# Optimization experiments

Measured on AMD Instinct MI355X. Metric: run time of the kernel, lower is better.

The kernel has to match this reference:

```python
import jax, jax.numpy as jnp
import numpy as np

B, S = 4096, 128
POS_RANK, DIR_RANK = 10, 4
WIDTH = 256
POS_DIM = POS_RANK * 6  # 60
DIR_DIM = DIR_RANK * 6  # 24
SKIPS = (4,)


def _pe(x, rank):
    # x: [N, 3] -> [N, 6*rank]; sin/cos of x scaled by 2^i for i in 0..rank-1
    freqs = (2.0 ** jnp.arange(rank)).astype(x.dtype)        # [L]
    xf = x[..., None] * freqs                                 # [N, 3, L]
    enc = jnp.concatenate([jnp.sin(xf), jnp.cos(xf)], axis=-1)  # [N, 3, 2L]
    return enc.reshape(x.shape[0], -1)


def _linear_init(key, fan_in, fan_out):
    k1, k2 = jax.random.split(key)
    bound = 1.0 / np.sqrt(fan_in)
    W = jax.random.uniform(k1, (fan_in, fan_out), jnp.float32, -bound, bound)
    b = jax.random.uniform(k2, (fan_out,), jnp.float32, -bound, bound)
    return W, b


def setup_inputs() -> dict:
    key = jax.random.key(0)
    ks = jax.random.split(key, 16)
    inp = {
        "input_pos": jax.random.normal(ks[0], (B, S, 3), jnp.float32),
        "input_dir": jax.random.normal(ks[1], (B, S, 3), jnp.float32),
    }
    # trunk layers: in-dims follow skip-concat structure
    in_dims = [POS_DIM] + [WIDTH + POS_DIM if (i in SKIPS) else WIDTH for i in range(7)]
    for i, d_in in enumerate(in_dims):
        W, b = _linear_init(ks[2 + i], d_in, WIDTH)
        inp[f"W{i}"] = W
        inp[f"b{i}"] = b
    inp["Wd"], inp["bd"] = _linear_init(ks[10], WIDTH, 1)
    inp["Wc0"], inp["bc0"] = _linear_init(ks[11], WIDTH + DIR_DIM, WIDTH // 2)
    inp["Wc1"], inp["bc1"] = _linear_init(ks[12], WIDTH // 2, 3)
    return inp


def reference(input_pos, input_dir,
              W0, b0, W1, b1, W2, b2, W3, b3, W4, b4, W5, b5, W6, b6, W7, b7,
              Wd, bd, Wc0, bc0, Wc1, bc1):
    Ws = [W0, W1, W2, W3, W4, W5, W6, W7]
    bs = [b0, b1, b2, b3, b4, b5, b6, b7]
    b, s, _ = input_pos.shape
    embed_pos = _pe(input_pos.reshape(-1, 3), POS_RANK)  # [N, 60]
    embed_dir = _pe(input_dir.reshape(-1, 3), DIR_RANK)  # [N, 24]
    hx = embed_pos
    for i, (W, bb) in enumerate(zip(Ws, bs)):
        hx = jax.nn.relu(hx @ W + bb)
        if i in SKIPS:
            hx = jnp.concatenate([hx, embed_pos], axis=1)
    density = (hx @ Wd + bd).reshape(b, s)
    dir_feat = jnp.concatenate([hx, embed_dir], axis=1)  # [N, 280]
    color = (jax.nn.relu(dir_feat @ Wc0 + bc0) @ Wc1 + bc1).reshape(b, s, 3)
    return density, color
```

## Files before the change

kernel.cpp:

```cpp
#include <hip/hip_runtime.h>
#include <hip/hip_bf16.h>

using bf16 = __bf16;
typedef __bf16 bf16x8 __attribute__((ext_vector_type(8)));
typedef __bf16 bf16x4 __attribute__((ext_vector_type(4)));
typedef float  f32x4  __attribute__((ext_vector_type(4)));

#define MFMA16(a, b, c) __builtin_amdgcn_mfma_f32_16x16x32_bf16((a), (b), (c), 0, 0, 0)

constexpr int P0  = 0;
constexpr int P1  = 16384;
constexpr int P2  = 81920;
constexpr int P3  = 147456;
constexpr int P4  = 212992;
constexpr int P5  = 278528;
constexpr int P6  = 360448;
constexpr int P7  = 425984;
constexpr int PD  = 491520;
constexpr int PC0 = 495616;
constexpr int PC1 = 532480;

constexpr int NPTS = 4096 * 128;
constexpr int MT = 128;
constexpr int PTILES = MT / 16;
constexpr int SH = 320;


struct PackArgs {
    const float* src[11];
    int K[11], N[11], Ntiles[11], tasks[11], dstoff[11];
};

__global__ void nerf_pack(PackArgs pa, bf16* __restrict__ dst) {
    int idx = blockIdx.x * 256 + threadIdx.x;
    for (int l = 0; l < 11; ++l) {
        if (idx < pa.tasks[l]) {
            const int lane = idx & 63;
            const int blk  = idx >> 6;
            const int nt   = blk % pa.Ntiles[l];
            const int kt   = blk / pa.Ntiles[l];
            const int kb   = kt * 32 + (lane >> 4) * 8;
            const int n    = nt * 16 + (lane & 15);
            const float* s = pa.src[l];
            const int K = pa.K[l], N = pa.N[l];
            bf16x8 v;
#pragma unroll
            for (int j = 0; j < 8; ++j) {
                int k = kb + j;
                v[j] = (bf16)((k < K && n < N) ? s[(size_t)k * N + n] : 0.f);
            }
            *(bf16x8*)(dst + pa.dstoff[l] + (size_t)idx * 8) = v;
            return;
        }
        idx -= pa.tasks[l];
    }
}

template <int KP, int N, bool RELU, int MODE, bool HAZARD, int COFF>
__device__ __forceinline__ void layer(bf16* H,
                                      const bf16* __restrict__ wp,
                                      const float* __restrict__ bias,
                                      float* __restrict__ gout, int m0) {
    constexpr int NW     = 8;
    constexpr int NTILES = N / 16;
    constexpr int NT_W   = (NTILES >= 16) ? 4 : ((NTILES >= 8) ? 2 : 1);
    constexpr int CG     = NTILES / NT_W;
    static_assert(CG <= NW && NW % CG == 0, "wave split");
    constexpr int NPG    = NW / CG;
    constexpr int PT_W   = PTILES / NPG;

    const int tid  = threadIdx.x;
    const int lane = tid & 63;
    const int w    = tid >> 6;
    const int l15  = lane & 15;
    const int quad = lane >> 4;
    const int swz  = l15 & 7;
    const int nt0  = (w % CG) * NT_W;
    const int pt0  = (w / CG) * PT_W;

    f32x4 acc[PT_W][NT_W];
    if constexpr (MODE == 0) {
#pragma unroll
        for (int nt = 0; nt < NT_W; ++nt) {
            f32x4 b4 = *(const f32x4*)(bias + (nt0 + nt) * 16 + quad * 4);
#pragma unroll
            for (int pt = 0; pt < PT_W; ++pt) acc[pt][nt] = b4;
        }
    } else if constexpr (MODE == 1) {
        const float bv = bias[0];
        f32x4 t = {bv, bv, bv, bv};
#pragma unroll
        for (int pt = 0; pt < PT_W; ++pt) acc[pt][0] = t;
    } else {
        f32x4 t = {bias[0], bias[1], bias[2], 0.f};
#pragma unroll
        for (int pt = 0; pt < PT_W; ++pt) acc[pt][0] = t;
    }

#pragma unroll 2
    for (int kt = 0; kt < KP / 32; ++kt) {
        bf16x8 wf[NT_W];
#pragma unroll
        for (int nt = 0; nt < NT_W; ++nt)
            wf[nt] = *(const bf16x8*)(wp + ((size_t)(kt * NTILES + nt0 + nt) * 64 + lane) * 8);
#pragma unroll
        for (int pt = 0; pt < PT_W; ++pt) {
            const int point = (pt0 + pt) * 16 + l15;
            const int chunk = (COFF >> 3) + kt * 4 + quad;
            bf16x8 af = *(const bf16x8*)(H + point * SH + ((chunk ^ swz) << 3));
#pragma unroll
            for (int nt = 0; nt < NT_W; ++nt)
                acc[pt][nt] = MFMA16(wf[nt], af, acc[pt][nt]);
        }
    }
    if (HAZARD) __syncthreads();

    if constexpr (MODE == 0) {
#pragma unroll
        for (int pt = 0; pt < PT_W; ++pt) {
            const int point = (pt0 + pt) * 16 + l15;
#pragma unroll
            for (int nt = 0; nt < NT_W; ++nt) {
                f32x4 a = acc[pt][nt];
                bf16x4 o;
#pragma unroll
                for (int r = 0; r < 4; ++r) {
                    float v = a[r];
                    if (RELU) v = v > 0.f ? v : 0.f;
                    o[r] = (bf16)v;
                }
                const int chunk = (nt0 + nt) * 2 + (quad >> 1);
                *(bf16x4*)(H + point * SH + ((chunk ^ swz) << 3) + (quad & 1) * 4) = o;
            }
        }
        __syncthreads();
    } else if constexpr (MODE == 1) {
        if (quad == 0) {
#pragma unroll
            for (int pt = 0; pt < PT_W; ++pt)
                gout[m0 + (pt0 + pt) * 16 + l15] = acc[pt][0][0];
        }
    } else {
        if (quad == 0) {
#pragma unroll
            for (int pt = 0; pt < PT_W; ++pt) {
                const size_t p3 = (size_t)(m0 + (pt0 + pt) * 16 + l15) * 3;
                gout[p3 + 0] = acc[pt][0][0];
                gout[p3 + 1] = acc[pt][0][1];
                gout[p3 + 2] = acc[pt][0][2];
            }
        }
    }
}

__global__ __launch_bounds__(512, 4)
void nerf_main(const float* __restrict__ pos, const float* __restrict__ dir,
               const float* __restrict__ b0, const float* __restrict__ b1,
               const float* __restrict__ b2, const float* __restrict__ b3,
               const float* __restrict__ b4, const float* __restrict__ b5,
               const float* __restrict__ b6, const float* __restrict__ b7,
               const float* __restrict__ bd, const float* __restrict__ bc0,
               const float* __restrict__ bc1,
               const bf16* __restrict__ wpk, float* __restrict__ out) {
    __shared__ __align__(16) bf16 H[MT * SH];

    const int m0 = blockIdx.x * MT;
    const int tid = threadIdx.x;

    {
        const int row = tid >> 2;
        const int sub = tid & 3;
        const int swz = row & 7;
        const size_t pb = (size_t)(m0 + row) * 3;
        float xs[3] = { pos[pb], pos[pb + 1], pos[pb + 2] };
#pragma unroll
        for (int h = 0; h < 2; ++h) {
            const int chunk = 32 + sub * 2 + h;
            bf16* dst = H + row * SH + ((chunk ^ swz) << 3);
#pragma unroll
            for (int j = 0; j < 8; ++j) {
                const int col = sub * 16 + h * 8 + j;
                float v = 0.f;
                if (col < 60) {
                    const int c = col / 20, rem = col % 20, s = rem / 10, i = rem % 10;
                    const float arg = xs[c] * (float)(1 << i);
                    v = s ? __cosf(arg) : __sinf(arg);
                }
                dst[j] = (bf16)v;
            }
        }
    }
    __syncthreads();

    layer<64,  256, true, 0, false, 256>(H, wpk + P0, b0, nullptr, m0);
    layer<256, 256, true, 0, true,  0  >(H, wpk + P1, b1, nullptr, m0);
    layer<256, 256, true, 0, true,  0  >(H, wpk + P2, b2, nullptr, m0);
    layer<256, 256, true, 0, true,  0  >(H, wpk + P3, b3, nullptr, m0);
    layer<256, 256, true, 0, true,  0  >(H, wpk + P4, b4, nullptr, m0);
    layer<320, 256, true, 0, true,  0  >(H, wpk + P5, b5, nullptr, m0);
    layer<256, 256, true, 0, true,  0  >(H, wpk + P6, b6, nullptr, m0);
    layer<256, 256, true, 0, true,  0  >(H, wpk + P7, b7, nullptr, m0);

    layer<256, 16, false, 1, false, 0>(H, wpk + PD, bd, out, m0);

    {
        const int row = tid >> 2;
        const int sub = tid & 3;
        const int swz = row & 7;
        const size_t db = (size_t)(m0 + row) * 3;
        float ds[3] = { dir[db], dir[db + 1], dir[db + 2] };
        const int chunk = 32 + sub;
        bf16* dst = H + row * SH + ((chunk ^ swz) << 3);
#pragma unroll
        for (int j = 0; j < 8; ++j) {
            const int col = sub * 8 + j;
            float v = 0.f;
            if (col < 24) {
                const int c = col / 8, rem = col % 8, s = rem / 4, i = rem % 4;
                const float arg = ds[c] * (float)(1 << i);
                v = s ? __cosf(arg) : __sinf(arg);
            }
            dst[j] = (bf16)v;
        }
    }
    __syncthreads();

    layer<288, 128, true, 0, true,  0>(H, wpk + PC0, bc0, nullptr, m0);
    layer<128, 16, false, 2, false, 0>(H, wpk + PC1, bc1, out + NPTS, m0);
}

__global__ void nerf_sentinel(float* __restrict__ out, float val) {
    if (threadIdx.x == 0 && blockIdx.x == 0) out[0] = val;
}

extern "C" void kernel_launch(void* const* d_in, const int* in_sizes, int n_in,
                              void* d_out, int out_size, void* d_ws, size_t ws_size,
                              hipStream_t stream) {
    static const int exp2[24] = {
        1572864, 1572864,
        15360, 256, 65536, 256, 65536, 256, 65536, 256,
        65536, 256, 80896, 256, 65536, 256, 65536, 256,
        256, 1, 35840, 128, 384, 3
    };
    int bad = -1;
    if (n_in != 24) bad = 99;
    else {
        for (int i = 0; i < 24; ++i)
            if (in_sizes[i] != exp2[i]) { bad = i; break; }
    }
    if (bad < 0 && out_size != NPTS * 4) bad = 97;
    if (bad >= 0) {
        nerf_sentinel<<<1, 64, 0, stream>>>((float*)d_out, 20000.f + 100.f * bad);
        return;
    }

    static const int wi[11] = {2, 4, 6, 8, 10, 12, 14, 16, 18, 20, 22};
    static const int Ks[11] = {60, 256, 256, 256, 256, 316, 256, 256, 256, 280, 128};
    static const int Ns[11] = {256, 256, 256, 256, 256, 256, 256, 256, 1, 128, 3};
    static const int Kp[11] = {64, 256, 256, 256, 256, 320, 256, 256, 256, 288, 128};
    static const int Np[11] = {256, 256, 256, 256, 256, 256, 256, 256, 16, 128, 16};

    PackArgs pa;
    int off = 0, total_tasks = 0;
    for (int l = 0; l < 11; ++l) {
        pa.src[l]    = (const float*)d_in[wi[l]];
        pa.K[l]      = Ks[l];
        pa.N[l]      = Ns[l];
        pa.Ntiles[l] = Np[l] / 16;
        pa.tasks[l]  = (Kp[l] / 32) * (Np[l] / 16) * 64;
        pa.dstoff[l] = off;
        off += pa.tasks[l] * 8;
        total_tasks += pa.tasks[l];
    }
    bf16* wpk = (bf16*)d_ws;

    nerf_pack<<<(total_tasks + 255) / 256, 256, 0, stream>>>(pa, wpk);

    nerf_main<<<NPTS / MT, 512, 0, stream>>>(
        (const float*)d_in[0], (const float*)d_in[1],
        (const float*)d_in[3], (const float*)d_in[5], (const float*)d_in[7],
        (const float*)d_in[9], (const float*)d_in[11], (const float*)d_in[13],
        (const float*)d_in[15], (const float*)d_in[17], (const float*)d_in[19],
        (const float*)d_in[21], (const float*)d_in[23],
        wpk, (float*)d_out);
}
```

Baseline: 586.0 us.

## Switch MLP layers from 16x16x32 to 32x32x16 bf16 MFMA tiles

Replaces the 16x16x32 MFMA with the 32x32x16 variant throughout the fused NeRF MLP. The weight packing, LDS fragment addressing, swizzle, bias initialisation and output write-back are reworked for 32-wide tiles. The larger instruction should reuse each loaded operand fragment across more output elements, cutting LDS and global fragment loads per FLOP. The costs are more accumulator registers per wave (16 floats per tile), idle waves in the narrow output layers, and a tricky swizzle scheme that has to stay consistent between the read and write paths.

```diff
diff --git a/kernel.cpp b/kernel.cpp
--- a/kernel.cpp
+++ b/kernel.cpp
@@ -5,8 +5,9 @@
 typedef __bf16 bf16x8 __attribute__((ext_vector_type(8)));
 typedef __bf16 bf16x4 __attribute__((ext_vector_type(4)));
 typedef float  f32x4  __attribute__((ext_vector_type(4)));
-
-#define MFMA16(a, b, c) __builtin_amdgcn_mfma_f32_16x16x32_bf16((a), (b), (c), 0, 0, 0)
+typedef float  f32x16 __attribute__((ext_vector_type(16)));
+
+#define MFMA32(a, b, c) __builtin_amdgcn_mfma_f32_32x32x16_bf16((a), (b), (c), 0, 0, 0)
 
 constexpr int P0  = 0;
 constexpr int P1  = 16384;
@@ -17,12 +18,12 @@
 constexpr int P6  = 360448;
 constexpr int P7  = 425984;
 constexpr int PD  = 491520;
-constexpr int PC0 = 495616;
-constexpr int PC1 = 532480;
+constexpr int PC0 = 499712;
+constexpr int PC1 = 536576;
 
 constexpr int NPTS = 4096 * 128;
 constexpr int MT = 128;
-constexpr int PTILES = MT / 16;
+constexpr int PTILES = MT / 32;
 constexpr int SH = 320;
 
 
@@ -39,8 +40,8 @@
             const int blk  = idx >> 6;
             const int nt   = blk % pa.Ntiles[l];
             const int kt   = blk / pa.Ntiles[l];
-            const int kb   = kt * 32 + (lane >> 4) * 8;
-            const int n    = nt * 16 + (lane & 15);
+            const int kb   = kt * 16 + ((lane >> 5) << 3);
+            const int n    = nt * 32 + (lane & 31);
             const float* s = pa.src[l];
             const int K = pa.K[l], N = pa.N[l];
             bf16x8 v;
@@ -61,56 +62,68 @@
                                       const bf16* __restrict__ wp,
                                       const float* __restrict__ bias,
                                       float* __restrict__ gout, int m0) {
-    constexpr int NW     = 8;
-    constexpr int NTILES = N / 16;
-    constexpr int NT_W   = (NTILES >= 16) ? 4 : ((NTILES >= 8) ? 2 : 1);
+    constexpr int NTILES = N / 32;
+    constexpr int NT_W   = (NTILES >= 2) ? 2 : 1;
     constexpr int CG     = NTILES / NT_W;
-    static_assert(CG <= NW && NW % CG == 0, "wave split");
-    constexpr int NPG    = NW / CG;
-    constexpr int PT_W   = PTILES / NPG;
+    constexpr int NPG    = 8 / CG;
+    constexpr int PT_W   = (PTILES + NPG - 1) / NPG;
+    constexpr int CB     = COFF >> 3;
 
     const int tid  = threadIdx.x;
     const int lane = tid & 63;
     const int w    = tid >> 6;
-    const int l15  = lane & 15;
-    const int quad = lane >> 4;
-    const int swz  = l15 & 7;
+    const int l31  = lane & 31;
+    const int hi   = lane >> 5;
     const int nt0  = (w % CG) * NT_W;
     const int pt0  = (w / CG) * PT_W;
-
-    f32x4 acc[PT_W][NT_W];
+    const int s15  = l31 & 15, s7 = l31 & 7;
+
+    f32x16 acc[PT_W][NT_W];
     if constexpr (MODE == 0) {
 #pragma unroll
         for (int nt = 0; nt < NT_W; ++nt) {
-            f32x4 b4 = *(const f32x4*)(bias + (nt0 + nt) * 16 + quad * 4);
-#pragma unroll
-            for (int pt = 0; pt < PT_W; ++pt) acc[pt][nt] = b4;
-        }
-    } else if constexpr (MODE == 1) {
-        const float bv = bias[0];
-        f32x4 t = {bv, bv, bv, bv};
-#pragma unroll
-        for (int pt = 0; pt < PT_W; ++pt) acc[pt][0] = t;
+#pragma unroll
+            for (int g = 0; g < 4; ++g) {
+                f32x4 b4 = *(const f32x4*)(bias + (nt0 + nt) * 32 + g * 8 + hi * 4);
+#pragma unroll
+                for (int pt = 0; pt < PT_W; ++pt) {
+                    acc[pt][nt][g * 4 + 0] = b4[0];
+                    acc[pt][nt][g * 4 + 1] = b4[1];
+                    acc[pt][nt][g * 4 + 2] = b4[2];
+                    acc[pt][nt][g * 4 + 3] = b4[3];
+                }
+            }
+        }
     } else {
-        f32x4 t = {bias[0], bias[1], bias[2], 0.f};
-#pragma unroll
-        for (int pt = 0; pt < PT_W; ++pt) acc[pt][0] = t;
-    }
-
-#pragma unroll 2
-    for (int kt = 0; kt < KP / 32; ++kt) {
+#pragma unroll
+        for (int pt = 0; pt < PT_W; ++pt)
+#pragma unroll
+            for (int r = 0; r < 16; ++r) {
+                const int chan = (r & 3) + 8 * (r >> 2) + 4 * hi;
+                float bv = 0.f;
+                if (MODE == 1) bv = (chan == 0) ? bias[0] : 0.f;
+                else           bv = (chan < 3) ? bias[chan] : 0.f;
+                acc[pt][0][r] = bv;
+            }
+    }
+
+#pragma unroll 4
+    for (int kt = 0; kt < KP / 16; ++kt) {
         bf16x8 wf[NT_W];
 #pragma unroll
         for (int nt = 0; nt < NT_W; ++nt)
             wf[nt] = *(const bf16x8*)(wp + ((size_t)(kt * NTILES + nt0 + nt) * 64 + lane) * 8);
+        const int c = CB + kt * 2 + hi;
+        const int swz = (CB + kt * 2 < 32) ? s15 : s7;
 #pragma unroll
         for (int pt = 0; pt < PT_W; ++pt) {
-            const int point = (pt0 + pt) * 16 + l15;
-            const int chunk = (COFF >> 3) + kt * 4 + quad;
-            bf16x8 af = *(const bf16x8*)(H + point * SH + ((chunk ^ swz) << 3));
-#pragma unroll
-            for (int nt = 0; nt < NT_W; ++nt)
-                acc[pt][nt] = MFMA16(wf[nt], af, acc[pt][nt]);
+            if (pt0 + pt < PTILES) {
+                const int point = (pt0 + pt) * 32 + l31;
+                bf16x8 af = *(const bf16x8*)(H + point * SH + ((c ^ swz) << 3));
+#pragma unroll
+                for (int nt = 0; nt < NT_W; ++nt)
+                    acc[pt][nt] = MFMA32(wf[nt], af, acc[pt][nt]);
+            }
         }
     }
     if (HAZARD) __syncthreads();
@@ -118,37 +131,33 @@
     if constexpr (MODE == 0) {
 #pragma unroll
         for (int pt = 0; pt < PT_W; ++pt) {
-            const int point = (pt0 + pt) * 16 + l15;
+            const int point = (pt0 + pt) * 32 + l31;
 #pragma unroll
             for (int nt = 0; nt < NT_W; ++nt) {
-                f32x4 a = acc[pt][nt];
-                bf16x4 o;
-#pragma unroll
-                for (int r = 0; r < 4; ++r) {
-                    float v = a[r];
-                    if (RELU) v = v > 0.f ? v : 0.f;
-                    o[r] = (bf16)v;
+#pragma unroll
+                for (int g = 0; g < 4; ++g) {
+                    bf16x4 o;
+#pragma unroll
+                    for (int r = 0; r < 4; ++r) {
+                        float v = acc[pt][nt][g * 4 + r];
+                        if (RELU) v = v > 0.f ? v : 0.f;
+                        o[r] = (bf16)v;
+                    }
+                    const int chunk = (nt0 + nt) * 4 + g;
+                    *(bf16x4*)(H + point * SH + ((chunk ^ s15) << 3) + hi * 4) = o;
                 }
-                const int chunk = (nt0 + nt) * 2 + (quad >> 1);
-                *(bf16x4*)(H + point * SH + ((chunk ^ swz) << 3) + (quad & 1) * 4) = o;
             }
         }
         __syncthreads();
     } else if constexpr (MODE == 1) {
-        if (quad == 0) {
-#pragma unroll
-            for (int pt = 0; pt < PT_W; ++pt)
-                gout[m0 + (pt0 + pt) * 16 + l15] = acc[pt][0][0];
-        }
+        if (hi == 0 && pt0 < PTILES)
+            gout[m0 + pt0 * 32 + l31] = acc[0][0][0];
     } else {
-        if (quad == 0) {
-#pragma unroll
-            for (int pt = 0; pt < PT_W; ++pt) {
-                const size_t p3 = (size_t)(m0 + (pt0 + pt) * 16 + l15) * 3;
-                gout[p3 + 0] = acc[pt][0][0];
-                gout[p3 + 1] = acc[pt][0][1];
-                gout[p3 + 2] = acc[pt][0][2];
-            }
+        if (hi == 0 && pt0 < PTILES) {
+            const size_t p3 = (size_t)(m0 + pt0 * 32 + l31) * 3;
+            gout[p3 + 0] = acc[0][0][0];
+            gout[p3 + 1] = acc[0][0][1];
+            gout[p3 + 2] = acc[0][0][2];
         }
     }
 }
@@ -201,7 +210,7 @@
     layer<256, 256, true, 0, true,  0  >(H, wpk + P6, b6, nullptr, m0);
     layer<256, 256, true, 0, true,  0  >(H, wpk + P7, b7, nullptr, m0);
 
-    layer<256, 16, false, 1, false, 0>(H, wpk + PD, bd, out, m0);
+    layer<256, 32, false, 1, false, 0>(H, wpk + PD, bd, out, m0);
 
     {
         const int row = tid >> 2;
@@ -226,7 +235,7 @@
     __syncthreads();
 
     layer<288, 128, true, 0, true,  0>(H, wpk + PC0, bc0, nullptr, m0);
-    layer<128, 16, false, 2, false, 0>(H, wpk + PC1, bc1, out + NPTS, m0);
+    layer<128, 32, false, 2, false, 0>(H, wpk + PC1, bc1, out + NPTS, m0);
 }
 
 __global__ void nerf_sentinel(float* __restrict__ out, float val) {
@@ -258,7 +267,7 @@
     static const int Ks[11] = {60, 256, 256, 256, 256, 316, 256, 256, 256, 280, 128};
     static const int Ns[11] = {256, 256, 256, 256, 256, 256, 256, 256, 1, 128, 3};
     static const int Kp[11] = {64, 256, 256, 256, 256, 320, 256, 256, 256, 288, 128};
-    static const int Np[11] = {256, 256, 256, 256, 256, 256, 256, 256, 16, 128, 16};
+    static const int Np[11] = {256, 256, 256, 256, 256, 256, 256, 256, 32, 128, 32};
 
     PackArgs pa;
     int off = 0, total_tasks = 0;
@@ -266,8 +275,8 @@
         pa.src[l]    = (const float*)d_in[wi[l]];
         pa.K[l]      = Ks[l];
         pa.N[l]      = Ns[l];
-        pa.Ntiles[l] = Np[l] / 16;
-        pa.tasks[l]  = (Kp[l] / 32) * (Np[l] / 16) * 64;
+        pa.Ntiles[l] = Np[l] / 32;
+        pa.tasks[l]  = (Kp[l] / 16) * (Np[l] / 32) * 64;
         pa.dstoff[l] = off;
         off += pa.tasks[l] * 8;
         total_tasks += pa.tasks[l];
```

After: 716.6 us. 22.3% more time.
